# Kernel optimization log

Measured on AMD Instinct MI355X. Metric: run time of the kernel, lower is better.

## Reference

```python
import jax, jax.numpy as jnp
import numpy as np

N, E, H, C = 50000, 800000, 4, 64
IN_DIM = 128
HID = H * C            # 256, concat output width
VH = C // 2            # 32, value-head hidden
OUT_DIM = 4
NEG_SLOPE = 0.2
LN_EPS = 1e-5


def setup_inputs() -> dict:
    key = jax.random.key(0)
    ks = iter(jax.random.split(key, 64))
    def nrm(shape, s=0.05):
        return jax.random.normal(next(ks), shape, jnp.float32) * s
    inp = {
        "x": jax.random.normal(next(ks), (N, IN_DIM), jnp.float32),
        "edge_src": jax.random.randint(next(ks), (E,), 0, N, dtype=jnp.int32),
        "edge_dst": jax.random.randint(next(ks), (E,), 0, N, dtype=jnp.int32),
        "proj_w": nrm((C, IN_DIM)),
        "proj_b": jnp.zeros((C,), jnp.float32),
    }
    in_dims = [C, HID, HID]
    out_feats = [HID, HID, C]
    for i in range(3):
        inp[f"w{i}"] = nrm((HID, in_dims[i]))
        inp[f"asrc{i}"] = nrm((H, C))
        inp[f"adst{i}"] = nrm((H, C))
        inp[f"b{i}"] = jnp.zeros((out_feats[i],), jnp.float32)
        inp[f"g{i}"] = jnp.ones((out_feats[i],), jnp.float32)
        inp[f"be{i}"] = jnp.zeros((out_feats[i],), jnp.float32)
    inp["vw1"] = nrm((VH, C)); inp["vb1"] = jnp.zeros((VH,), jnp.float32)
    inp["vw2"] = nrm((OUT_DIM, VH)); inp["vb2"] = jnp.zeros((OUT_DIM,), jnp.float32)
    return inp


def _layer_norm(x, g, b):
    mu = x.mean(-1, keepdims=True)
    var = ((x - mu) ** 2).mean(-1, keepdims=True)
    return (x - mu) * jax.lax.rsqrt(var + LN_EPS) * g + b


def _gat_conv(x, src, dst, w, a_s, a_d, bias, concat):
    # x: [N, in_dim] -> h: [N, H, C]
    n = x.shape[0]
    h = (x @ w.T).reshape(n, H, C)
    asrc = jnp.einsum('nhc,hc->nh', h, a_s)  # [N, H]
    adst = jnp.einsum('nhc,hc->nh', h, a_d)
    # PyG default add_self_loops=True
    loop = jnp.arange(n, dtype=src.dtype)
    src_f = jnp.concatenate([src, loop])
    dst_f = jnp.concatenate([dst, loop])
    alpha = jax.nn.leaky_relu(asrc[src_f] + adst[dst_f], NEG_SLOPE)  # [E+N, H]
    # segment softmax over incoming edges of each destination node
    amax = jax.ops.segment_max(alpha, dst_f, num_segments=n)
    ex = jnp.exp(alpha - amax[dst_f])
    denom = jax.ops.segment_sum(ex, dst_f, num_segments=n)
    coef = ex / (denom[dst_f] + 1e-16)
    out = jax.ops.segment_sum(h[src_f] * coef[:, :, None], dst_f, num_segments=n)
    out = out.reshape(n, H * C) if concat else out.mean(axis=1)
    return out + bias


def _gat_layer(x, src, dst, w, a_s, a_d, bias, g, be, concat):
    # GATConv -> LayerNorm -> ELU (dropout is identity in eval)
    return jax.nn.elu(_layer_norm(_gat_conv(x, src, dst, w, a_s, a_d, bias, concat), g, be))


def reference(x, edge_src, edge_dst, proj_w, proj_b,
              w0, asrc0, adst0, b0, g0, be0,
              w1, asrc1, adst1, b1, g1, be1,
              w2, asrc2, adst2, b2, g2, be2,
              vw1, vb1, vw2, vb2):
    h = jax.nn.elu(x @ proj_w.T + proj_b)
    h = _gat_layer(h, edge_src, edge_dst, w0, asrc0, adst0, b0, g0, be0, True)
    h = _gat_layer(h, edge_src, edge_dst, w1, asrc1, adst1, b1, g1, be1, True)
    h = _gat_layer(h, edge_src, edge_dst, w2, asrc2, adst2, b2, g2, be2, False)
    v = jax.nn.elu(h @ vw1.T + vb1)
    return v @ vw2.T + vb2
```

## Files before the change

kernel.cpp:

```cpp
#include <hip/hip_runtime.h>

typedef unsigned short u16;
typedef u16 u16x4 __attribute__((ext_vector_type(4)));
typedef short short8 __attribute__((ext_vector_type(8)));
typedef float f32x4 __attribute__((ext_vector_type(4)));

__device__ __forceinline__ float elu_f(float x) { return x > 0.f ? x : expm1f(x); }
__device__ __forceinline__ float lrelu_f(float x) { return x > 0.f ? x : 0.2f * x; }

__device__ __forceinline__ u16 f2b(float f) {
  union { float f; unsigned u; } v; v.f = f;
  unsigned r = v.u + 0x7FFF + ((v.u >> 16) & 1);
  return (u16)(r >> 16);
}
__device__ __forceinline__ float b2f(u16 u) {
  union { unsigned u; float f; } v; v.u = ((unsigned)u) << 16; return v.f;
}

__global__ void deg_count_k(const int* __restrict__ src, const int* __restrict__ dst,
                            int E, int n, int* __restrict__ deg) {
  int e = blockIdx.x * blockDim.x + threadIdx.x;
  if (e < E) {
    atomicAdd(&deg[dst[e]], 1);
  } else if (e < E + n) {
    atomicAdd(&deg[e - E], 1);
  }
}

__global__ __launch_bounds__(256) void block_sum_k(const int* __restrict__ deg,
                                                   int* __restrict__ bsum, int n) {
  int i = blockIdx.x * 256 + threadIdx.x;
  int v = (i < n) ? deg[i] : 0;
#pragma unroll
  for (int off = 1; off < 64; off <<= 1) v += __shfl_xor(v, off);
  __shared__ int ws[4];
  if ((threadIdx.x & 63) == 0) ws[threadIdx.x >> 6] = v;
  __syncthreads();
  if (threadIdx.x == 0) bsum[blockIdx.x] = ws[0] + ws[1] + ws[2] + ws[3];
}

__global__ void scan_bsum_k(int* __restrict__ bsum, int nb) {
  __shared__ int s[1024];
  int tid = threadIdx.x;
  int v = (tid < nb) ? bsum[tid] : 0;
  s[tid] = v;
  __syncthreads();
  for (int off = 1; off < 1024; off <<= 1) {
    int t = (tid >= off) ? s[tid - off] : 0;
    __syncthreads();
    s[tid] += t;
    __syncthreads();
  }
  if (tid < nb) bsum[tid] = s[tid] - v;
}

__global__ __launch_bounds__(256) void block_scan_k(const int* __restrict__ deg,
                                                    const int* __restrict__ bsum,
                                                    int* __restrict__ rowptr,
                                                    int* __restrict__ cursor, int n) {
  int i = blockIdx.x * 256 + threadIdx.x;
  int lane = threadIdx.x & 63, w = threadIdx.x >> 6;
  int v = (i < n) ? deg[i] : 0;
  int x = v;
#pragma unroll
  for (int off = 1; off < 64; off <<= 1) {
    int t = __shfl_up(x, off);
    if (lane >= off) x += t;
  }
  __shared__ int ws[4];
  if (lane == 63) ws[w] = x;
  __syncthreads();
  int add = bsum[blockIdx.x];
  for (int j = 0; j < w; ++j) add += ws[j];
  int excl = x - v + add;
  if (i < n) {
    cursor[i] = excl;
    rowptr[i + 1] = excl + v;
  }
  if (i == 0) rowptr[0] = 0;
}

__global__ void scatter_k(const int* __restrict__ src, const int* __restrict__ dst,
                          int E, int n, int* __restrict__ cursor,
                          int* __restrict__ col, int* __restrict__ dst2) {
  int e = blockIdx.x * blockDim.x + threadIdx.x;
  if (e < E) {
    int d = dst[e];
    int pos = atomicAdd(&cursor[d], 1);
    col[pos] = src[e];
    dst2[pos] = d;
  } else if (e < E + n) {
    int d = e - E;
    int pos = atomicAdd(&cursor[d], 1);
    col[pos] = d;
    dst2[pos] = d;
  }
}

__global__ __launch_bounds__(256) void cvt_all_k(const float* __restrict__ x, u16* __restrict__ xb,
                                                 int nx8,
                                                 const float* __restrict__ pw,
                                                 const float* __restrict__ w0,
                                                 const float* __restrict__ w1,
                                                 const float* __restrict__ w2,
                                                 u16* __restrict__ dp, u16* __restrict__ d0,
                                                 u16* __restrict__ d1, u16* __restrict__ d2) {
  int i = blockIdx.x * 256 + threadIdx.x;
  if (i < nx8) {
    int j = i * 8;
    float4 a = *reinterpret_cast<const float4*>(&x[j]);
    float4 b = *reinterpret_cast<const float4*>(&x[j + 4]);
    u16x4 o0, o1;
    o0.x = f2b(a.x); o0.y = f2b(a.y); o0.z = f2b(a.z); o0.w = f2b(a.w);
    o1.x = f2b(b.x); o1.y = f2b(b.y); o1.z = f2b(b.z); o1.w = f2b(b.w);
    *reinterpret_cast<u16x4*>(&xb[j]) = o0;
    *reinterpret_cast<u16x4*>(&xb[j + 4]) = o1;
  } else {
    int j = i - nx8;
    if (j < 8192) dp[j] = f2b(pw[j]);
    else if (j < 24576) d0[j - 8192] = f2b(w0[j - 8192]);
    else if (j < 90112) d1[j - 24576] = f2b(w1[j - 24576]);
    else if (j < 155648) d2[j - 90112] = f2b(w2[j - 90112]);
  }
}

template <int BIASELU, int ATTN>
__global__ __launch_bounds__(256) void gemm_bf16_k(const u16* __restrict__ A, int lda,
                                                   const u16* __restrict__ W,
                                                   const float* __restrict__ bias,
                                                   u16* __restrict__ Cb, int ldc,
                                                   int n, int K, int ncols,
                                                   const float* __restrict__ a_sv,
                                                   const float* __restrict__ a_dv,
                                                   float* __restrict__ asrcN,
                                                   float* __restrict__ adstN) {
  __shared__ int4 Abuf[1024];
  __shared__ int4 Bbuf[1024];
  char* Asb = (char*)Abuf;
  char* Bsb = (char*)Bbuf;
  const int t = threadIdx.x;
  const int lane = t & 63, w = t >> 6;
  const int wrow = w >> 1, wcol = w & 1;
  const int row0 = blockIdx.x * 128, col0 = blockIdx.y * 128;
  f32x4 acc[4][4];
#pragma unroll
  for (int m = 0; m < 4; ++m)
#pragma unroll
    for (int nf = 0; nf < 4; ++nf) acc[m][nf] = (f32x4){0.f, 0.f, 0.f, 0.f};

  for (int k0 = 0; k0 < K; k0 += 64) {
#pragma unroll
    for (int i = 0; i < 4; ++i) {
      int ci = i * 256 + t;
      int r = ci >> 3;
      int b = (ci & 7) << 4;
      int sw = b ^ ((r & 7) << 4);
      int ar = row0 + r; ar = ar < n ? ar : n - 1;
      int4 av = *reinterpret_cast<const int4*>(&A[(size_t)ar * lda + k0 + (b >> 1)]);
      *reinterpret_cast<int4*>(Asb + r * 128 + sw) = av;
      int wr = col0 + r; wr = wr < ncols ? wr : ncols - 1;
      int4 wv = *reinterpret_cast<const int4*>(&W[(size_t)wr * K + k0 + (b >> 1)]);
      *reinterpret_cast<int4*>(Bsb + r * 128 + sw) = wv;
    }
    __syncthreads();
#pragma unroll
    for (int ks = 0; ks < 2; ++ks) {
      short8 af[4], bf[4];
      int kb = ks * 64 + ((lane >> 4) << 4);
#pragma unroll
      for (int m = 0; m < 4; ++m) {
        int r = wrow * 64 + m * 16 + (lane & 15);
        af[m] = *reinterpret_cast<const short8*>(Asb + r * 128 + (kb ^ ((r & 7) << 4)));
      }
#pragma unroll
      for (int nf = 0; nf < 4; ++nf) {
        int r = wcol * 64 + nf * 16 + (lane & 15);
        bf[nf] = *reinterpret_cast<const short8*>(Bsb + r * 128 + (kb ^ ((r & 7) << 4)));
      }
#pragma unroll
      for (int m = 0; m < 4; ++m)
#pragma unroll
        for (int nf = 0; nf < 4; ++nf)
          acc[m][nf] = __builtin_amdgcn_mfma_f32_16x16x32_bf16(af[m], bf[nf], acc[m][nf], 0, 0, 0);
    }
    __syncthreads();
  }
#pragma unroll
  for (int m = 0; m < 4; ++m) {
#pragma unroll
    for (int j = 0; j < 4; ++j) {
      int rg = row0 + wrow * 64 + m * 16 + (lane >> 4) * 4 + j;
      if (rg >= n) continue;
#pragma unroll
      for (int nf = 0; nf < 4; ++nf) {
        int cg = col0 + wcol * 64 + nf * 16 + (lane & 15);
        if (cg >= ncols) continue;
        float v = acc[m][nf][j];
        if (BIASELU) v = elu_f(v + bias[cg]);
        Cb[(size_t)rg * ldc + cg] = f2b(v);
      }
    }
  }
  if (ATTN) {
    int h = (col0 >> 6) + wcol;
    int ch = lane & 15;
    float as_c[4], ad_c[4];
#pragma unroll
    for (int nf = 0; nf < 4; ++nf) {
      as_c[nf] = a_sv[h * 64 + nf * 16 + ch];
      ad_c[nf] = a_dv[h * 64 + nf * 16 + ch];
    }
#pragma unroll
    for (int m = 0; m < 4; ++m) {
#pragma unroll
      for (int j = 0; j < 4; ++j) {
        float ps = 0.f, pd = 0.f;
#pragma unroll
        for (int nf = 0; nf < 4; ++nf) {
          float v = acc[m][nf][j];
          ps += v * as_c[nf];
          pd += v * ad_c[nf];
        }
#pragma unroll
        for (int off = 1; off < 16; off <<= 1) {
          ps += __shfl_xor(ps, off);
          pd += __shfl_xor(pd, off);
        }
        int rg = row0 + wrow * 64 + m * 16 + (lane >> 4) * 4 + j;
        if ((lane & 15) == 0 && rg < n) {
          asrcN[(size_t)rg * 4 + h] = ps;
          adstN[(size_t)rg * 4 + h] = pd;
        }
      }
    }
  }
}

__global__ __launch_bounds__(256) void edge_ex_k(const int* __restrict__ col,
                                                 const int* __restrict__ dst2,
                                                 const float* __restrict__ asrcN,
                                                 const float* __restrict__ adstN,
                                                 float* __restrict__ ex, int EE) {
  int t = blockIdx.x * 256 + threadIdx.x;
  if (t >= EE * 4) return;
  int e = t >> 2, h = t & 3;
  int s = col[e], d = dst2[e];
  float a = asrcN[(size_t)s * 4 + h] + adstN[(size_t)d * 4 + h];
  ex[t] = __expf(lrelu_f(a));
}

template <int MODE>
__global__ __launch_bounds__(256) void gat_agg2_k(const u16* __restrict__ feat,
                                                  const float* __restrict__ ex,
                                                  const int* __restrict__ rowptr,
                                                  const int* __restrict__ col,
                                                  const float* __restrict__ bias,
                                                  const float* __restrict__ g,
                                                  const float* __restrict__ be,
                                                  void* __restrict__ out, int n) {
  int wave = threadIdx.x >> 6, lane = threadIdx.x & 63;
  int node = blockIdx.x * 4 + wave;
  if (node >= n) return;
  int h = lane >> 4;
  int s0 = rowptr[node], s1 = rowptr[node + 1];
  float ax = 0.f, ay = 0.f, az = 0.f, aw = 0.f, den = 0.f;
  int e = s0;
  for (; e + 4 <= s1; e += 4) {
    int sa = col[e + 0], sb = col[e + 1], sc = col[e + 2], sd = col[e + 3];
    float xa = ex[(size_t)(e + 0) * 4 + h];
    float xb = ex[(size_t)(e + 1) * 4 + h];
    float xc = ex[(size_t)(e + 2) * 4 + h];
    float xd = ex[(size_t)(e + 3) * 4 + h];
    u16x4 fa = *reinterpret_cast<const u16x4*>(&feat[(size_t)sa * 256 + lane * 4]);
    u16x4 fb = *reinterpret_cast<const u16x4*>(&feat[(size_t)sb * 256 + lane * 4]);
    u16x4 fc = *reinterpret_cast<const u16x4*>(&feat[(size_t)sc * 256 + lane * 4]);
    u16x4 fd = *reinterpret_cast<const u16x4*>(&feat[(size_t)sd * 256 + lane * 4]);
    den += (xa + xb) + (xc + xd);
    ax += xa * b2f(fa.x) + xb * b2f(fb.x) + xc * b2f(fc.x) + xd * b2f(fd.x);
    ay += xa * b2f(fa.y) + xb * b2f(fb.y) + xc * b2f(fc.y) + xd * b2f(fd.y);
    az += xa * b2f(fa.z) + xb * b2f(fb.z) + xc * b2f(fc.z) + xd * b2f(fd.z);
    aw += xa * b2f(fa.w) + xb * b2f(fb.w) + xc * b2f(fc.w) + xd * b2f(fd.w);
  }
  for (; e < s1; ++e) {
    int s = col[e];
    float x = ex[(size_t)e * 4 + h];
    den += x;
    u16x4 f = *reinterpret_cast<const u16x4*>(&feat[(size_t)s * 256 + lane * 4]);
    ax += x * b2f(f.x); ay += x * b2f(f.y); az += x * b2f(f.z); aw += x * b2f(f.w);
  }
  float inv = 1.f / den;
  ax *= inv; ay *= inv; az *= inv; aw *= inv;

  if (MODE == 0) {
    float4 b4 = *reinterpret_cast<const float4*>(&bias[lane * 4]);
    float vx = ax + b4.x, vy = ay + b4.y, vz = az + b4.z, vw = aw + b4.w;
    float s = vx + vy + vz + vw;
#pragma unroll
    for (int off = 1; off < 64; off <<= 1) s += __shfl_xor(s, off);
    float mu = s * (1.f / 256.f);
    float dx = vx - mu, dy = vy - mu, dz = vz - mu, dw = vw - mu;
    float q = dx * dx + dy * dy + dz * dz + dw * dw;
#pragma unroll
    for (int off = 1; off < 64; off <<= 1) q += __shfl_xor(q, off);
    float inv2 = rsqrtf(q * (1.f / 256.f) + 1e-5f);
    float4 gg = *reinterpret_cast<const float4*>(&g[lane * 4]);
    float4 bb = *reinterpret_cast<const float4*>(&be[lane * 4]);
    u16x4 o;
    o.x = f2b(elu_f(dx * inv2 * gg.x + bb.x));
    o.y = f2b(elu_f(dy * inv2 * gg.y + bb.y));
    o.z = f2b(elu_f(dz * inv2 * gg.z + bb.z));
    o.w = f2b(elu_f(dw * inv2 * gg.w + bb.w));
    u16* rowb = (u16*)out + (size_t)node * 256;
    *reinterpret_cast<u16x4*>(&rowb[lane * 4]) = o;
  } else {
    ax += __shfl_xor(ax, 16); ax += __shfl_xor(ax, 32);
    ay += __shfl_xor(ay, 16); ay += __shfl_xor(ay, 32);
    az += __shfl_xor(az, 16); az += __shfl_xor(az, 32);
    aw += __shfl_xor(aw, 16); aw += __shfl_xor(aw, 32);
    int qd = lane & 15;
    float4 b4 = *reinterpret_cast<const float4*>(&bias[qd * 4]);
    float vx = 0.25f * ax + b4.x, vy = 0.25f * ay + b4.y;
    float vz = 0.25f * az + b4.z, vw = 0.25f * aw + b4.w;
    float s = vx + vy + vz + vw;
#pragma unroll
    for (int off = 1; off < 64; off <<= 1) s += __shfl_xor(s, off);
    float mu = s * (1.f / 256.f);
    float dx = vx - mu, dy = vy - mu, dz = vz - mu, dw = vw - mu;
    float q = dx * dx + dy * dy + dz * dz + dw * dw;
#pragma unroll
    for (int off = 1; off < 64; off <<= 1) q += __shfl_xor(q, off);
    float inv2 = rsqrtf(q * (1.f / 256.f) + 1e-5f);
    if (lane < 16) {
      float4 gg = *reinterpret_cast<const float4*>(&g[qd * 4]);
      float4 bb = *reinterpret_cast<const float4*>(&be[qd * 4]);
      float4 o;
      o.x = elu_f(dx * inv2 * gg.x + bb.x);
      o.y = elu_f(dy * inv2 * gg.y + bb.y);
      o.z = elu_f(dz * inv2 * gg.z + bb.z);
      o.w = elu_f(dw * inv2 * gg.w + bb.w);
      *reinterpret_cast<float4*>(&((float*)out)[(size_t)node * 64 + qd * 4]) = o;
    }
  }
}

__global__ __launch_bounds__(256) void value_head_k(const float* __restrict__ hh,
                                                    const float* __restrict__ vw1,
                                                    const float* __restrict__ vb1,
                                                    const float* __restrict__ vw2,
                                                    const float* __restrict__ vb2,
                                                    float* __restrict__ out, int n) {
  __shared__ float w1s[32 * 65];
  __shared__ float hs[4][64];
  __shared__ float vs[4][33];
  int tid = threadIdx.x;
  for (int i = tid; i < 2048; i += 256) w1s[(i >> 6) * 65 + (i & 63)] = vw1[i];
  int wave = tid >> 6, lane = tid & 63;
  int node = blockIdx.x * 4 + wave;
  int nc = node < n ? node : n - 1;
  hs[wave][lane] = hh[(size_t)nc * 64 + lane];
  __syncthreads();
  int j = lane & 31, half = lane >> 5;
  float p = 0.f;
#pragma unroll
  for (int c = 0; c < 32; ++c) p += hs[wave][half * 32 + c] * w1s[j * 65 + half * 32 + c];
  p += __shfl_xor(p, 32);
  float v = elu_f(p + vb1[j]);
  if (half == 0) vs[wave][j] = v;
  __syncthreads();
  if (lane < 4 && node < n) {
    float o = vb2[lane];
#pragma unroll
    for (int jj = 0; jj < 32; ++jj) o += vs[wave][jj] * vw2[lane * 32 + jj];
    out[(size_t)node * 4 + lane] = o;
  }
}

extern "C" void kernel_launch(void* const* d_in, const int* in_sizes, int n_in,
                              void* d_out, int out_size, void* d_ws, size_t ws_size,
                              hipStream_t stream) {
  const float* x      = (const float*)d_in[0];
  const int*   esrc   = (const int*)d_in[1];
  const int*   edst   = (const int*)d_in[2];
  const float* proj_w = (const float*)d_in[3];
  const float* proj_b = (const float*)d_in[4];
  const float* w[3]   = {(const float*)d_in[5],  (const float*)d_in[11], (const float*)d_in[17]};
  const float* a_s[3] = {(const float*)d_in[6],  (const float*)d_in[12], (const float*)d_in[18]};
  const float* a_d[3] = {(const float*)d_in[7],  (const float*)d_in[13], (const float*)d_in[19]};
  const float* bb[3]  = {(const float*)d_in[8],  (const float*)d_in[14], (const float*)d_in[20]};
  const float* gg[3]  = {(const float*)d_in[9],  (const float*)d_in[15], (const float*)d_in[21]};
  const float* be[3]  = {(const float*)d_in[10], (const float*)d_in[16], (const float*)d_in[22]};
  const float* vw1 = (const float*)d_in[23];
  const float* vb1 = (const float*)d_in[24];
  const float* vw2 = (const float*)d_in[25];
  const float* vb2 = (const float*)d_in[26];
  float* outp = (float*)d_out;

  const int n = in_sizes[0] / 128;
  const int E = in_sizes[1];
  const int EE = E + n;
  const int nbl = (n + 255) / 256;

  char* p = (char*)d_ws;
  auto alloc = [&](size_t bytes) { char* r = p; p += (bytes + 255) & ~(size_t)255; return r; };
  u16*   hA    = (u16*)alloc((size_t)n * 512);
  u16*   featB = (u16*)alloc((size_t)n * 512);
  float* ex    = (float*)alloc((size_t)EE * 16);
  float* asrcN = (float*)alloc((size_t)n * 16);
  float* adstN = (float*)alloc((size_t)n * 16);
  u16* wbp = (u16*)alloc(64 * 128 * 2);
  u16* wb[3];
  wb[0] = (u16*)alloc(256 * 64 * 2);
  wb[1] = (u16*)alloc(256 * 256 * 2);
  wb[2] = (u16*)alloc(256 * 256 * 2);
  int* deg    = (int*)alloc((size_t)n * 4);
  int* rowptr = (int*)alloc((size_t)(n + 1) * 4);
  int* cursor = (int*)alloc((size_t)n * 4);
  int* col    = (int*)alloc((size_t)EE * 4);
  int* dst2   = (int*)alloc((size_t)EE * 4);
  int* bsum   = (int*)alloc((size_t)nbl * 4);
  float* hfinal = (float*)hA;

  hipMemsetAsync(deg, 0, (size_t)n * sizeof(int), stream);
  deg_count_k<<<(EE + 255) / 256, 256, 0, stream>>>(esrc, edst, E, n, deg);
  block_sum_k<<<nbl, 256, 0, stream>>>(deg, bsum, n);
  scan_bsum_k<<<1, 1024, 0, stream>>>(bsum, nbl);
  block_scan_k<<<nbl, 256, 0, stream>>>(deg, bsum, rowptr, cursor, n);
  scatter_k<<<(EE + 255) / 256, 256, 0, stream>>>(esrc, edst, E, n, cursor, col, dst2);

  const int nx8 = n * 16;
  cvt_all_k<<<(nx8 + 155648 + 255) / 256, 256, 0, stream>>>(x, featB, nx8, proj_w, w[0], w[1], w[2],
                                                            wbp, wb[0], wb[1], wb[2]);

  const int nb4 = (n + 3) / 4;
  const int nbg = (n + 127) / 128;
  dim3 blk(256);

  gemm_bf16_k<1, 0><<<dim3(nbg, 1), blk, 0, stream>>>(featB, 128, wbp, proj_b, hA, 256, n, 128, 64,
                                                      nullptr, nullptr, nullptr, nullptr);

  const int Kin[3] = {64, 256, 256};
  for (int i = 0; i < 3; ++i) {
    gemm_bf16_k<0, 1><<<dim3(nbg, 2), blk, 0, stream>>>(hA, 256, wb[i], nullptr, featB, 256, n,
                                                        Kin[i], 256, a_s[i], a_d[i], asrcN, adstN);
    edge_ex_k<<<((size_t)EE * 4 + 255) / 256, 256, 0, stream>>>(col, dst2, asrcN, adstN, ex, EE);
    if (i < 2) {
      gat_agg2_k<0><<<nb4, blk, 0, stream>>>(featB, ex, rowptr, col, bb[i], gg[i], be[i], (void*)hA, n);
    } else {
      gat_agg2_k<1><<<nb4, blk, 0, stream>>>(featB, ex, rowptr, col, bb[i], gg[i], be[i], (void*)hfinal, n);
    }
  }

  value_head_k<<<nb4, blk, 0, stream>>>(hfinal, vw1, vb1, vw2, vb2, outp, n);
}
```

Measured before the change: 462.7 us.

## Transpose edge scores per head, widen GAT GEMM tile, unroll aggregation by eight

The per-layer GEMM now runs as a 512-thread block covering all 256 output columns, so each A tile is loaded once instead of twice across two column blocks. The edge-score kernel handles one edge per thread with float4 loads and writes scores head-major, so aggregation reads for each head are contiguous. The aggregation loop is unrolled to eight edges to keep more gathers in flight. The cost is more shared memory and registers per block, which can lower occupancy.

```diff
diff --git a/kernel.cpp b/kernel.cpp
--- a/kernel.cpp
+++ b/kernel.cpp
@@ -124,16 +124,12 @@
   }
 }
 
-template <int BIASELU, int ATTN>
+template <int BIASELU>
 __global__ __launch_bounds__(256) void gemm_bf16_k(const u16* __restrict__ A, int lda,
                                                    const u16* __restrict__ W,
                                                    const float* __restrict__ bias,
                                                    u16* __restrict__ Cb, int ldc,
-                                                   int n, int K, int ncols,
-                                                   const float* __restrict__ a_sv,
-                                                   const float* __restrict__ a_dv,
-                                                   float* __restrict__ asrcN,
-                                                   float* __restrict__ adstN) {
+                                                   int n, int K, int ncols) {
   __shared__ int4 Abuf[1024];
   __shared__ int4 Bbuf[1024];
   char* Asb = (char*)Abuf;
@@ -201,8 +197,86 @@
       }
     }
   }
-  if (ATTN) {
-    int h = (col0 >> 6) + wcol;
+}
+
+__global__ __launch_bounds__(512) void gemm2_k(const u16* __restrict__ A, int lda,
+                                               const u16* __restrict__ W,
+                                               u16* __restrict__ Cb,
+                                               int n, int K,
+                                               const float* __restrict__ a_sv,
+                                               const float* __restrict__ a_dv,
+                                               float* __restrict__ asrcN,
+                                               float* __restrict__ adstN) {
+  __shared__ char Asb[128 * 128];
+  __shared__ char Bsb[256 * 128];
+  const int t = threadIdx.x;
+  const int lane = t & 63, w = t >> 6;
+  const int wrow = w >> 2, wcol = w & 3;
+  const int row0 = blockIdx.x * 128;
+  f32x4 acc[4][4];
+#pragma unroll
+  for (int m = 0; m < 4; ++m)
+#pragma unroll
+    for (int nf = 0; nf < 4; ++nf) acc[m][nf] = (f32x4){0.f, 0.f, 0.f, 0.f};
+
+  for (int k0 = 0; k0 < K; k0 += 64) {
+#pragma unroll
+    for (int i = 0; i < 2; ++i) {
+      int ci = i * 512 + t;
+      int r = ci >> 3;
+      int b = (ci & 7) << 4;
+      int sw = b ^ ((r & 7) << 4);
+      int ar = row0 + r; ar = ar < n ? ar : n - 1;
+      int4 av = *reinterpret_cast<const int4*>(&A[(size_t)ar * lda + k0 + (b >> 1)]);
+      *reinterpret_cast<int4*>(Asb + r * 128 + sw) = av;
+    }
+#pragma unroll
+    for (int i = 0; i < 4; ++i) {
+      int ci = i * 512 + t;
+      int r = ci >> 3;
+      int b = (ci & 7) << 4;
+      int sw = b ^ ((r & 7) << 4);
+      int4 wv = *reinterpret_cast<const int4*>(&W[(size_t)r * K + k0 + (b >> 1)]);
+      *reinterpret_cast<int4*>(Bsb + r * 128 + sw) = wv;
+    }
+    __syncthreads();
+#pragma unroll
+    for (int ks = 0; ks < 2; ++ks) {
+      short8 af[4], bf[4];
+      int kb = ks * 64 + ((lane >> 4) << 4);
+#pragma unroll
+      for (int m = 0; m < 4; ++m) {
+        int r = wrow * 64 + m * 16 + (lane & 15);
+        af[m] = *reinterpret_cast<const short8*>(Asb + r * 128 + (kb ^ ((r & 7) << 4)));
+      }
+#pragma unroll
+      for (int nf = 0; nf < 4; ++nf) {
+        int r = wcol * 64 + nf * 16 + (lane & 15);
+        bf[nf] = *reinterpret_cast<const short8*>(Bsb + r * 128 + (kb ^ ((r & 7) << 4)));
+      }
+#pragma unroll
+      for (int m = 0; m < 4; ++m)
+#pragma unroll
+        for (int nf = 0; nf < 4; ++nf)
+          acc[m][nf] = __builtin_amdgcn_mfma_f32_16x16x32_bf16(af[m], bf[nf], acc[m][nf], 0, 0, 0);
+    }
+    __syncthreads();
+  }
+#pragma unroll
+  for (int m = 0; m < 4; ++m) {
+#pragma unroll
+    for (int j = 0; j < 4; ++j) {
+      int rg = row0 + wrow * 64 + m * 16 + (lane >> 4) * 4 + j;
+      if (rg >= n) continue;
+#pragma unroll
+      for (int nf = 0; nf < 4; ++nf) {
+        int cg = wcol * 64 + nf * 16 + (lane & 15);
+        Cb[(size_t)rg * 256 + cg] = f2b(acc[m][nf][j]);
+      }
+    }
+  }
+  {
+    int h = wcol;
     int ch = lane & 15;
     float as_c[4], ad_c[4];
 #pragma unroll
@@ -236,22 +310,25 @@
   }
 }
 
-__global__ __launch_bounds__(256) void edge_ex_k(const int* __restrict__ col,
-                                                 const int* __restrict__ dst2,
-                                                 const float* __restrict__ asrcN,
-                                                 const float* __restrict__ adstN,
-                                                 float* __restrict__ ex, int EE) {
-  int t = blockIdx.x * 256 + threadIdx.x;
-  if (t >= EE * 4) return;
-  int e = t >> 2, h = t & 3;
+__global__ __launch_bounds__(256) void edge_ex2_k(const int* __restrict__ col,
+                                                  const int* __restrict__ dst2,
+                                                  const float* __restrict__ asrcN,
+                                                  const float* __restrict__ adstN,
+                                                  float* __restrict__ exT, int eep, int EE) {
+  int e = blockIdx.x * 256 + threadIdx.x;
+  if (e >= EE) return;
   int s = col[e], d = dst2[e];
-  float a = asrcN[(size_t)s * 4 + h] + adstN[(size_t)d * 4 + h];
-  ex[t] = __expf(lrelu_f(a));
+  float4 as = *reinterpret_cast<const float4*>(&asrcN[(size_t)s * 4]);
+  float4 ad = *reinterpret_cast<const float4*>(&adstN[(size_t)d * 4]);
+  exT[e]            = __expf(lrelu_f(as.x + ad.x));
+  exT[eep + e]      = __expf(lrelu_f(as.y + ad.y));
+  exT[2 * eep + e]  = __expf(lrelu_f(as.z + ad.z));
+  exT[3 * eep + e]  = __expf(lrelu_f(as.w + ad.w));
 }
 
 template <int MODE>
-__global__ __launch_bounds__(256) void gat_agg2_k(const u16* __restrict__ feat,
-                                                  const float* __restrict__ ex,
+__global__ __launch_bounds__(256) void gat_agg4_k(const u16* __restrict__ feat,
+                                                  const float* __restrict__ exT, int eep,
                                                   const int* __restrict__ rowptr,
                                                   const int* __restrict__ col,
                                                   const float* __restrict__ bias,
@@ -262,28 +339,49 @@
   int node = blockIdx.x * 4 + wave;
   if (node >= n) return;
   int h = lane >> 4;
+  const float* exh = exT + (size_t)h * eep;
   int s0 = rowptr[node], s1 = rowptr[node + 1];
   float ax = 0.f, ay = 0.f, az = 0.f, aw = 0.f, den = 0.f;
   int e = s0;
+  for (; e + 8 <= s1; e += 8) {
+    int p0 = col[e + 0], p1 = col[e + 1], p2 = col[e + 2], p3 = col[e + 3];
+    int q0 = col[e + 4], q1 = col[e + 5], q2 = col[e + 6], q3 = col[e + 7];
+    float u0 = exh[e + 0], u1 = exh[e + 1], u2 = exh[e + 2], u3 = exh[e + 3];
+    float v0 = exh[e + 4], v1 = exh[e + 5], v2 = exh[e + 6], v3 = exh[e + 7];
+    u16x4 fp0 = *reinterpret_cast<const u16x4*>(&feat[(size_t)p0 * 256 + lane * 4]);
+    u16x4 fp1 = *reinterpret_cast<const u16x4*>(&feat[(size_t)p1 * 256 + lane * 4]);
+    u16x4 fp2 = *reinterpret_cast<const u16x4*>(&feat[(size_t)p2 * 256 + lane * 4]);
+    u16x4 fp3 = *reinterpret_cast<const u16x4*>(&feat[(size_t)p3 * 256 + lane * 4]);
+    u16x4 fq0 = *reinterpret_cast<const u16x4*>(&feat[(size_t)q0 * 256 + lane * 4]);
+    u16x4 fq1 = *reinterpret_cast<const u16x4*>(&feat[(size_t)q1 * 256 + lane * 4]);
+    u16x4 fq2 = *reinterpret_cast<const u16x4*>(&feat[(size_t)q2 * 256 + lane * 4]);
+    u16x4 fq3 = *reinterpret_cast<const u16x4*>(&feat[(size_t)q3 * 256 + lane * 4]);
+    den += ((u0 + u1) + (u2 + u3)) + ((v0 + v1) + (v2 + v3));
+    ax += u0 * b2f(fp0.x) + u1 * b2f(fp1.x) + u2 * b2f(fp2.x) + u3 * b2f(fp3.x);
+    ay += u0 * b2f(fp0.y) + u1 * b2f(fp1.y) + u2 * b2f(fp2.y) + u3 * b2f(fp3.y);
+    az += u0 * b2f(fp0.z) + u1 * b2f(fp1.z) + u2 * b2f(fp2.z) + u3 * b2f(fp3.z);
+    aw += u0 * b2f(fp0.w) + u1 * b2f(fp1.w) + u2 * b2f(fp2.w) + u3 * b2f(fp3.w);
+    ax += v0 * b2f(fq0.x) + v1 * b2f(fq1.x) + v2 * b2f(fq2.x) + v3 * b2f(fq3.x);
+    ay += v0 * b2f(fq0.y) + v1 * b2f(fq1.y) + v2 * b2f(fq2.y) + v3 * b2f(fq3.y);
+    az += v0 * b2f(fq0.z) + v1 * b2f(fq1.z) + v2 * b2f(fq2.z) + v3 * b2f(fq3.z);
+    aw += v0 * b2f(fq0.w) + v1 * b2f(fq1.w) + v2 * b2f(fq2.w) + v3 * b2f(fq3.w);
+  }
   for (; e + 4 <= s1; e += 4) {
-    int sa = col[e + 0], sb = col[e + 1], sc = col[e + 2], sd = col[e + 3];
-    float xa = ex[(size_t)(e + 0) * 4 + h];
-    float xb = ex[(size_t)(e + 1) * 4 + h];
-    float xc = ex[(size_t)(e + 2) * 4 + h];
-    float xd = ex[(size_t)(e + 3) * 4 + h];
-    u16x4 fa = *reinterpret_cast<const u16x4*>(&feat[(size_t)sa * 256 + lane * 4]);
-    u16x4 fb = *reinterpret_cast<const u16x4*>(&feat[(size_t)sb * 256 + lane * 4]);
-    u16x4 fc = *reinterpret_cast<const u16x4*>(&feat[(size_t)sc * 256 + lane * 4]);
-    u16x4 fd = *reinterpret_cast<const u16x4*>(&feat[(size_t)sd * 256 + lane * 4]);
-    den += (xa + xb) + (xc + xd);
-    ax += xa * b2f(fa.x) + xb * b2f(fb.x) + xc * b2f(fc.x) + xd * b2f(fd.x);
-    ay += xa * b2f(fa.y) + xb * b2f(fb.y) + xc * b2f(fc.y) + xd * b2f(fd.y);
-    az += xa * b2f(fa.z) + xb * b2f(fb.z) + xc * b2f(fc.z) + xd * b2f(fd.z);
-    aw += xa * b2f(fa.w) + xb * b2f(fb.w) + xc * b2f(fc.w) + xd * b2f(fd.w);
+    int p0 = col[e + 0], p1 = col[e + 1], p2 = col[e + 2], p3 = col[e + 3];
+    float u0 = exh[e + 0], u1 = exh[e + 1], u2 = exh[e + 2], u3 = exh[e + 3];
+    u16x4 fp0 = *reinterpret_cast<const u16x4*>(&feat[(size_t)p0 * 256 + lane * 4]);
+    u16x4 fp1 = *reinterpret_cast<const u16x4*>(&feat[(size_t)p1 * 256 + lane * 4]);
+    u16x4 fp2 = *reinterpret_cast<const u16x4*>(&feat[(size_t)p2 * 256 + lane * 4]);
+    u16x4 fp3 = *reinterpret_cast<const u16x4*>(&feat[(size_t)p3 * 256 + lane * 4]);
+    den += (u0 + u1) + (u2 + u3);
+    ax += u0 * b2f(fp0.x) + u1 * b2f(fp1.x) + u2 * b2f(fp2.x) + u3 * b2f(fp3.x);
+    ay += u0 * b2f(fp0.y) + u1 * b2f(fp1.y) + u2 * b2f(fp2.y) + u3 * b2f(fp3.y);
+    az += u0 * b2f(fp0.z) + u1 * b2f(fp1.z) + u2 * b2f(fp2.z) + u3 * b2f(fp3.z);
+    aw += u0 * b2f(fp0.w) + u1 * b2f(fp1.w) + u2 * b2f(fp2.w) + u3 * b2f(fp3.w);
   }
   for (; e < s1; ++e) {
     int s = col[e];
-    float x = ex[(size_t)e * 4 + h];
+    float x = exh[e];
     den += x;
     u16x4 f = *reinterpret_cast<const u16x4*>(&feat[(size_t)s * 256 + lane * 4]);
     ax += x * b2f(f.x); ay += x * b2f(f.y); az += x * b2f(f.z); aw += x * b2f(f.w);
@@ -398,13 +496,14 @@
   const int n = in_sizes[0] / 128;
   const int E = in_sizes[1];
   const int EE = E + n;
+  const int eep = (EE + 255) & ~255;
   const int nbl = (n + 255) / 256;
 
   char* p = (char*)d_ws;
   auto alloc = [&](size_t bytes) { char* r = p; p += (bytes + 255) & ~(size_t)255; return r; };
   u16*   hA    = (u16*)alloc((size_t)n * 512);
   u16*   featB = (u16*)alloc((size_t)n * 512);
-  float* ex    = (float*)alloc((size_t)EE * 16);
+  float* exT   = (float*)alloc((size_t)eep * 16);
   float* asrcN = (float*)alloc((size_t)n * 16);
   float* adstN = (float*)alloc((size_t)n * 16);
   u16* wbp = (u16*)alloc(64 * 128 * 2);
@@ -435,18 +534,17 @@
   const int nbg = (n + 127) / 128;
   dim3 blk(256);
 
-  gemm_bf16_k<1, 0><<<dim3(nbg, 1), blk, 0, stream>>>(featB, 128, wbp, proj_b, hA, 256, n, 128, 64,
-                                                      nullptr, nullptr, nullptr, nullptr);
+  gemm_bf16_k<1><<<dim3(nbg, 1), blk, 0, stream>>>(featB, 128, wbp, proj_b, hA, 256, n, 128, 64);
 
   const int Kin[3] = {64, 256, 256};
   for (int i = 0; i < 3; ++i) {
-    gemm_bf16_k<0, 1><<<dim3(nbg, 2), blk, 0, stream>>>(hA, 256, wb[i], nullptr, featB, 256, n,
-                                                        Kin[i], 256, a_s[i], a_d[i], asrcN, adstN);
-    edge_ex_k<<<((size_t)EE * 4 + 255) / 256, 256, 0, stream>>>(col, dst2, asrcN, adstN, ex, EE);
+    gemm2_k<<<nbg, 512, 0, stream>>>(hA, 256, wb[i], featB, n, Kin[i],
+                                     a_s[i], a_d[i], asrcN, adstN);
+    edge_ex2_k<<<(EE + 255) / 256, 256, 0, stream>>>(col, dst2, asrcN, adstN, exT, eep, EE);
     if (i < 2) {
-      gat_agg2_k<0><<<nb4, blk, 0, stream>>>(featB, ex, rowptr, col, bb[i], gg[i], be[i], (void*)hA, n);
+      gat_agg4_k<0><<<nb4, blk, 0, stream>>>(featB, exT, eep, rowptr, col, bb[i], gg[i], be[i], (void*)hA, n);
     } else {
-      gat_agg2_k<1><<<nb4, blk, 0, stream>>>(featB, ex, rowptr, col, bb[i], gg[i], be[i], (void*)hfinal, n);
+      gat_agg4_k<1><<<nb4, blk, 0, stream>>>(featB, exT, eep, rowptr, col, bb[i], gg[i], be[i], (void*)hfinal, n);
     }
   }
 
```

New measurement: 426.1 us. 7.9% less time.
